# Kernel optimization log

Hardware: AMD Instinct MI355X
Metric: run time of the kernel (lower is better)

Reference implementation:

```python
import jax, jax.numpy as jnp
import numpy as np
import math

B, S, D = 2, 2048, 512
H = 8
DEPTH = D // H
MAX_REL = 1024
NEG_INF = -1.0e9


def skew(t):
    # t: (..., r, c). Pad a zero column on the left, reshape to move relative
    # logits into their absolute positions (Music Transformer skew trick).
    r, c = t.shape[-2], t.shape[-1]
    padded = jnp.pad(t, [(0, 0)] * (t.ndim - 1) + [(1, 0)])
    s = padded.reshape(-1, c + 1, r)[:, 1:]
    return s.reshape(t.shape)


def setup_inputs() -> dict:
    key = jax.random.key(0)
    ks = jax.random.split(key, 12)
    sc = 1.0 / math.sqrt(D)
    return {
        "q": jax.random.normal(ks[0], (B, S, D), jnp.float32),
        "k": jax.random.normal(ks[1], (B, S, D), jnp.float32),
        "v": jax.random.normal(ks[2], (B, S, D), jnp.float32),
        "mask": jax.random.randint(ks[3], (B, 1, S, S), 0, 2, jnp.int32),
        "Wq_w": jax.random.normal(ks[4], (D, D), jnp.float32) * sc,
        "Wq_b": jnp.zeros((D,), jnp.float32),
        "Wk_w": jax.random.normal(ks[5], (D, D), jnp.float32) * sc,
        "Wk_b": jnp.zeros((D,), jnp.float32),
        "Wv_w": jax.random.normal(ks[6], (D, D), jnp.float32) * sc,
        "Wv_b": jnp.zeros((D,), jnp.float32),
        "E": jax.random.normal(ks[7], (MAX_REL, D), jnp.float32),
        "Wo_w": jax.random.normal(ks[8], (D, D), jnp.float32) * sc,
        "Wo_b": jnp.zeros((D,), jnp.float32),
    }


def reference(q, k, v, mask, Wq_w, Wq_b, Wk_w, Wk_b, Wv_w, Wv_b, E, Wo_w, Wo_b):
    # Linear projections (torch Linear: x @ W^T + b)
    qp = q @ Wq_w.T + Wq_b
    kp = k @ Wk_w.T + Wk_b
    vp = v @ Wv_w.T + Wv_b

    # Required relative position embeddings for seq_len S (S >= MAX_REL here:
    # repeat E[0] for the first S-MAX_REL positions, then the full table).
    n_rep = max(0, S - MAX_REL)
    e = jnp.concatenate([jnp.tile(E[0:1], (n_rep, 1)), E[max(0, MAX_REL - S):]], axis=0)  # (S, D)

    # Split heads: (B,S,D)->(B,H,S,depth); e: (S,D)->(H,S,depth)
    qh = qp.reshape(B, S, H, DEPTH).transpose(0, 2, 1, 3)
    kh = kp.reshape(B, S, H, DEPTH).transpose(0, 2, 1, 3)
    vh = vp.reshape(B, S, H, DEPTH).transpose(0, 2, 1, 3)
    eh = e.reshape(S, H, DEPTH).transpose(1, 0, 2)

    QKt = jnp.einsum('bhqd,bhkd->bhqk', qh, kh)
    Srel = skew(jnp.einsum('bhqd,hkd->bhqk', qh, eh))
    logits = (QKt + Srel) / math.sqrt(DEPTH)
    logits = logits + mask.astype(logits.dtype) * NEG_INF
    attn = jnp.einsum('bhqk,bhkd->bhqd', jax.nn.softmax(logits, axis=-1), vh)

    # Merge heads and output projection
    out = attn.transpose(0, 2, 1, 3).reshape(B, S, D)
    return out @ Wo_w.T + Wo_b
```

## Files before the change

kernel.cpp:

```cpp
#include <hip/hip_runtime.h>
#include <hip/hip_bf16.h>

#define BB 2
#define SS 2048
#define DD 512
#define HH 8
#define DP 64
#define MR 1024

typedef __attribute__((ext_vector_type(8))) short bf16x8;
typedef __attribute__((ext_vector_type(4))) float floatx4;

static __device__ __forceinline__ unsigned short f2b(float x) {
    __hip_bfloat16 h = __float2bfloat16(x);
    return *reinterpret_cast<unsigned short*>(&h);
}
static __device__ __forceinline__ float b2f(unsigned short u) {
    __hip_bfloat16 h = *reinterpret_cast<__hip_bfloat16*>(&u);
    return __bfloat162float(h);
}
static __device__ __forceinline__ void gll16(const void* g, void* l) {
    __builtin_amdgcn_global_load_lds(
        (const __attribute__((address_space(1))) void*)g,
        (__attribute__((address_space(3))) void*)l, 16, 0, 0);
}
static __device__ __forceinline__ int xoff(int ks, int quad, int row) {
    return (((ks * 4 + quad) ^ (row & 7)) * 16);
}

__global__ __launch_bounds__(256) void prep_kernel(
    const float* __restrict__ Wq, const float* __restrict__ Wk,
    const float* __restrict__ Wv, const float* __restrict__ Wo,
    const float* __restrict__ E,  const float* __restrict__ q,
    const float* __restrict__ k,  const float* __restrict__ v,
    const int* __restrict__ mask,
    unsigned short* __restrict__ Wqb, unsigned short* __restrict__ Wkb,
    unsigned short* __restrict__ Wvb, unsigned short* __restrict__ Wob,
    unsigned short* __restrict__ Eb,  unsigned short* __restrict__ qb16,
    unsigned short* __restrict__ kb16, unsigned short* __restrict__ vb16,
    unsigned long long* __restrict__ bits)
{
    const int blk = blockIdx.x;
    if (blk < 7680) {
        const int gid = blk * 256 + threadIdx.x;
        const float* src; unsigned short* dst; int off;
        if      (gid < 65536)   { src = Wq; dst = Wqb;  off = gid; }
        else if (gid < 131072)  { src = Wk; dst = Wkb;  off = gid - 65536; }
        else if (gid < 196608)  { src = Wv; dst = Wvb;  off = gid - 131072; }
        else if (gid < 262144)  { src = Wo; dst = Wob;  off = gid - 196608; }
        else if (gid < 393216)  { src = E;  dst = Eb;   off = gid - 262144; }
        else if (gid < 917504)  { src = q;  dst = qb16; off = gid - 393216; }
        else if (gid < 1441792) { src = k;  dst = kb16; off = gid - 917504; }
        else                    { src = v;  dst = vb16; off = gid - 1441792; }
        float4 x = ((const float4*)src)[off];
        ushort4 u; u.x = f2b(x.x); u.y = f2b(x.y); u.z = f2b(x.z); u.w = f2b(x.w);
        ((ushort4*)dst)[off] = u;
    } else {
        const size_t wid = (size_t)(blk - 7680) * 4 + (threadIdx.x >> 6);
        const int lane = threadIdx.x & 63;
        const int mv = mask[wid * 64 + lane];
        unsigned long long bal = __ballot(mv != 0);
        if (lane == 0) bits[wid] = bal;
    }
}

__global__ __launch_bounds__(256) void gemm_proj(
    const unsigned short* __restrict__ Xq, const unsigned short* __restrict__ Xk,
    const unsigned short* __restrict__ Xv,
    const unsigned short* __restrict__ Wqb, const unsigned short* __restrict__ Wkb,
    const unsigned short* __restrict__ Wvb,
    const float* __restrict__ bq, const float* __restrict__ bk,
    const float* __restrict__ bv,
    unsigned short* __restrict__ qp, unsigned short* __restrict__ kp,
    unsigned short* __restrict__ vpT)
{
    const int z = blockIdx.z;
    const unsigned short* A  = (z == 0) ? Xq : (z == 1) ? Xk : Xv;
    const unsigned short* Wb = (z == 0) ? Wqb : (z == 1) ? Wkb : Wvb;
    const float* bias        = (z == 0) ? bq : (z == 1) ? bk : bv;

    __shared__ __align__(16) char parena[16384];
    char* AsB = parena;
    char* WsB = parena + 8192;
    const int t = threadIdx.x, lane = t & 63, w = t >> 6;
    const int quad = lane >> 4, l15 = lane & 15;
    const int wm = w >> 1, wn = w & 1;
    const int m0 = blockIdx.x * 64, n0 = blockIdx.y * 64;

    int srow[2], scol[2];
#pragma unroll
    for (int i = 0; i < 2; i++) {
        const int p = (w * 2 + i) * 64 + lane;
        srow[i] = p >> 3; scol[i] = (p & 7) ^ (srow[i] & 7);
    }

    floatx4 acc[2][2];
#pragma unroll
    for (int mi = 0; mi < 2; mi++)
#pragma unroll
        for (int ni = 0; ni < 2; ni++)
            acc[mi][ni] = (floatx4){0.f, 0.f, 0.f, 0.f};

    for (int k0 = 0; k0 < 512; k0 += 64) {
        if (k0) __syncthreads();
#pragma unroll
        for (int i = 0; i < 2; i++) {
            gll16(A + (size_t)(m0 + srow[i]) * 512 + k0 + scol[i] * 8,
                  AsB + (w * 2 + i) * 1024);
            gll16(Wb + (size_t)(n0 + srow[i]) * 512 + k0 + scol[i] * 8,
                  WsB + (w * 2 + i) * 1024);
        }
        __syncthreads();
#pragma unroll
        for (int ks = 0; ks < 2; ks++) {
            bf16x8 a[2], bb[2];
#pragma unroll
            for (int mi = 0; mi < 2; mi++) {
                const int row = wm * 32 + mi * 16 + l15;
                a[mi] = *(const bf16x8*)(AsB + row * 128 + xoff(ks, quad, row));
            }
#pragma unroll
            for (int ni = 0; ni < 2; ni++) {
                const int row = wn * 32 + ni * 16 + l15;
                bb[ni] = *(const bf16x8*)(WsB + row * 128 + xoff(ks, quad, row));
            }
#pragma unroll
            for (int mi = 0; mi < 2; mi++)
#pragma unroll
                for (int ni = 0; ni < 2; ni++)
                    acc[mi][ni] = __builtin_amdgcn_mfma_f32_16x16x32_bf16(
                        a[mi], bb[ni], acc[mi][ni], 0, 0, 0);
        }
    }

    if (z < 2) {
        unsigned short* Out = (z == 0) ? qp : kp;
#pragma unroll
        for (int ni = 0; ni < 2; ni++) {
            const int n = n0 + wn * 32 + ni * 16 + l15;
            const float bvl = bias[n];
#pragma unroll
            for (int mi = 0; mi < 2; mi++)
#pragma unroll
                for (int r = 0; r < 4; r++) {
                    const size_t m = (size_t)(m0 + wm * 32 + mi * 16 + quad * 4 + r);
                    Out[m * 512 + n] = f2b(acc[mi][ni][r] + bvl);
                }
        }
    } else {
        __syncthreads();
        unsigned short* Ls = (unsigned short*)parena;
#pragma unroll
        for (int ni = 0; ni < 2; ni++) {
            const int dcol = wn * 32 + ni * 16 + l15;
            const float bvl = bias[n0 + dcol];
#pragma unroll
            for (int mi = 0; mi < 2; mi++)
#pragma unroll
                for (int r = 0; r < 4; r++) {
                    const int srw = wm * 32 + mi * 16 + quad * 4 + r;
                    Ls[dcol * 72 + srw] = f2b(acc[mi][ni][r] + bvl);
                }
        }
        __syncthreads();
        const int bb2 = blockIdx.x >> 5, s0 = (blockIdx.x & 31) * 64, hh = blockIdx.y;
        const int drow = t >> 2, sc8 = (t & 3) * 8;
#pragma unroll
        for (int half = 0; half < 2; half++) {
            *(uint4*)&vpT[((size_t)(bb2 * 8 + hh) * 64 + drow) * SS + s0 + half * 32 + sc8] =
                *(const uint4*)&Ls[drow * 72 + half * 32 + sc8];
        }
    }
}

__global__ __launch_bounds__(256) void gemm_out(
    const unsigned short* __restrict__ A, const unsigned short* __restrict__ Wb,
    const float* __restrict__ bias, float* __restrict__ Out)
{
    __shared__ __align__(16) char parena[12288];
    char* AsB = parena;
    char* WsB = parena + 4096;
    const int t = threadIdx.x, lane = t & 63, w = t >> 6;
    const int quad = lane >> 4, l15 = lane & 15;
    const int wm = w >> 1, wn = w & 1;
    const int m0 = blockIdx.x * 32, n0 = blockIdx.y * 64;

    const int pa = w * 64 + lane;
    const int arow = pa >> 3, acol = (pa & 7) ^ (arow & 7);
    int wrow[2], wcol[2];
#pragma unroll
    for (int i = 0; i < 2; i++) {
        const int c = w * 2 + i;
        const int p = c * 64 + lane;
        wrow[i] = p >> 3; wcol[i] = (p & 7) ^ (wrow[i] & 7);
    }

    floatx4 acc[2];
    acc[0] = (floatx4){0.f, 0.f, 0.f, 0.f};
    acc[1] = (floatx4){0.f, 0.f, 0.f, 0.f};

    for (int k0 = 0; k0 < 512; k0 += 64) {
        if (k0) __syncthreads();
        gll16(A + (size_t)(m0 + arow) * 512 + k0 + acol * 8, AsB + w * 1024);
#pragma unroll
        for (int i = 0; i < 2; i++)
            gll16(Wb + (size_t)(n0 + wrow[i]) * 512 + k0 + wcol[i] * 8,
                  WsB + (w * 2 + i) * 1024);
        __syncthreads();
#pragma unroll
        for (int ks = 0; ks < 2; ks++) {
            bf16x8 a0 = *(const bf16x8*)(AsB + (wm * 16 + l15) * 128 + xoff(ks, quad, l15));
            bf16x8 b0 = *(const bf16x8*)(WsB + (wn * 32 + l15) * 128 + xoff(ks, quad, l15));
            bf16x8 b1 = *(const bf16x8*)(WsB + (wn * 32 + 16 + l15) * 128 + xoff(ks, quad, l15));
            acc[0] = __builtin_amdgcn_mfma_f32_16x16x32_bf16(a0, b0, acc[0], 0, 0, 0);
            acc[1] = __builtin_amdgcn_mfma_f32_16x16x32_bf16(a0, b1, acc[1], 0, 0, 0);
        }
    }
#pragma unroll
    for (int ct = 0; ct < 2; ct++) {
        const int n = n0 + wn * 32 + ct * 16 + l15;
        const float bvl = bias[n];
#pragma unroll
        for (int r = 0; r < 4; r++) {
            const size_t m = (size_t)(m0 + wm * 16 + quad * 4 + r);
            Out[m * 512 + n] = acc[ct][r] + bvl;
        }
    }
}

__global__ __launch_bounds__(256) void relg_kernel(
    const unsigned short* __restrict__ qp, const unsigned short* __restrict__ Eb,
    unsigned short* __restrict__ G)
{
    __shared__ unsigned short Ls[64 * 72];
    const int t = threadIdx.x, lane = t & 63, w = t >> 6;
    const int quad = lane >> 4, l15 = lane & 15;
    const int bh = blockIdx.z, b = bh >> 3, h = bh & 7;
    const int i0b = blockIdx.x * 64, t0 = blockIdx.y * 64;

    const unsigned short* Ar = qp + ((size_t)b * SS + i0b + w * 16 + l15) * DD + h * DP;
    bf16x8 a0 = *(const bf16x8*)(Ar + quad * 8);
    bf16x8 a1 = *(const bf16x8*)(Ar + 32 + quad * 8);

    floatx4 acc[4];
#pragma unroll
    for (int ct = 0; ct < 4; ct++) acc[ct] = (floatx4){0.f, 0.f, 0.f, 0.f};
#pragma unroll
    for (int ct = 0; ct < 4; ct++) {
        const unsigned short* Br = Eb + (size_t)(t0 + ct * 16 + l15) * DD + h * DP;
        bf16x8 b0 = *(const bf16x8*)(Br + quad * 8);
        bf16x8 b1 = *(const bf16x8*)(Br + 32 + quad * 8);
        acc[ct] = __builtin_amdgcn_mfma_f32_16x16x32_bf16(a0, b0, acc[ct], 0, 0, 0);
        acc[ct] = __builtin_amdgcn_mfma_f32_16x16x32_bf16(a1, b1, acc[ct], 0, 0, 0);
    }
#pragma unroll
    for (int ct = 0; ct < 4; ct++)
#pragma unroll
        for (int r = 0; r < 4; r++)
            Ls[(w * 16 + quad * 4 + r) * 72 + ct * 16 + l15] = f2b(acc[ct][r]);
    __syncthreads();
#pragma unroll
    for (int p = 0; p < 2; p++) {
        const int idx = p * 256 + t;
        const int row = idx >> 3, c8 = (idx & 7) * 8;
        *(uint4*)&G[((size_t)bh * SS + i0b + row) * MR + t0 + c8] =
            *(const uint4*)&Ls[row * 72 + c8];
    }
}

struct RelPF { ushort4 hi; ushort4 lo; int path; };

static __device__ __forceinline__ void rel_issue(
    const unsigned short* __restrict__ pdiag, int i0w, int k0, int quad,
    RelPF pf[2])
{
#pragma unroll
    for (int ct = 0; ct < 2; ct++) {
        const int k0c = k0 + ct * 16;
        const int gj0 = k0c + quad * 4;
        const int dmax = i0w + 15 - k0c;
        const int dmin = i0w - (k0c + 15);
        int path;
        if (dmin >= MR) path = 0;
        else if (dmin >= 0 && dmax <= MR - 1) path = 1;
        else if (dmax <= -2 && dmin >= -(MR + 1)) path = 2;
        else if (dmax <= -(MR + 2)) path = 3;
        else path = 4;
        pf[ct].path = path;
        if (path == 1 || path == 4) {
            const unsigned short* p = pdiag + 1023 + gj0;
            pf[ct].hi.x = p[0]; pf[ct].hi.y = p[1];
            pf[ct].hi.z = p[2]; pf[ct].hi.w = p[3];
        }
        if (path == 3 || path == 4) {
            const unsigned short* p = pdiag + max(gj0 - 2, 0);
            pf[ct].lo.x = p[0]; pf[ct].lo.y = p[1];
            pf[ct].lo.z = p[2]; pf[ct].lo.w = p[3];
        }
    }
}

static __device__ __forceinline__ void rel_convert(
    const RelPF& pf, int gi, int k0c, int quad,
    float d0a, float d0b, float relc[4])
{
    const int path = pf.path;
    if (path == 0) {
        relc[0] = relc[1] = relc[2] = relc[3] = d0a;
    } else if (path == 1) {
        relc[0] = b2f(pf.hi.x); relc[1] = b2f(pf.hi.y);
        relc[2] = b2f(pf.hi.z); relc[3] = b2f(pf.hi.w);
    } else if (path == 2) {
        relc[0] = relc[1] = relc[2] = relc[3] = d0b;
    } else if (path == 3) {
        relc[0] = b2f(pf.lo.x); relc[1] = b2f(pf.lo.y);
        relc[2] = b2f(pf.lo.z); relc[3] = b2f(pf.lo.w);
    } else {
        const int gj0 = k0c + quad * 4;
        const unsigned short hv[4] = {pf.hi.x, pf.hi.y, pf.hi.z, pf.hi.w};
        const unsigned short lv[4] = {pf.lo.x, pf.lo.y, pf.lo.z, pf.lo.w};
#pragma unroll
        for (int r = 0; r < 4; r++) {
            const int dd = gi - (gj0 + r);
            float rl;
            if (dd >= MR) rl = d0a;
            else if (dd >= 0) rl = b2f(hv[r]);
            else if (dd == -1) rl = 0.0f;
            else if (dd >= -(MR + 1)) rl = d0b;
            else rl = b2f(lv[r]);
            relc[r] = rl;
        }
    }
}

__global__ __launch_bounds__(256, 4) void attn_kernel(
    const unsigned short* __restrict__ qp, const unsigned short* __restrict__ kp,
    const unsigned short* __restrict__ vpT, const unsigned int* __restrict__ mb32,
    const unsigned short* __restrict__ G, unsigned short* __restrict__ ao)
{
    __shared__ __align__(16) char smem[38016];
    const int t = threadIdx.x, lane = t & 63, w = t >> 6;
    const int quad = lane >> 4, l15 = lane & 15;
    const int wr = w >> 1, kh = w & 1;
    const int bh = blockIdx.y, b = bh >> 3, h = bh & 7;
    const int i0w = blockIdx.x * 32 + wr * 16;
    const int gi = i0w + l15;

    const unsigned short* kb = kp + (size_t)b * SS * DD + h * DP;
    const unsigned short* vb = vpT + (size_t)bh * DP * SS;
    const unsigned short* Gb = G + (size_t)bh * SS * MR;
    const unsigned int* mrow32 = mb32 + ((size_t)b * SS + gi) * 64;

    const unsigned short* qrow = qp + ((size_t)b * SS + gi) * DD + h * DP;
    bf16x8 qf0 = *(const bf16x8*)(qrow + quad * 8);
    bf16x8 qf1 = *(const bf16x8*)(qrow + 32 + quad * 8);

    const unsigned short* pdiag = Gb + (size_t)gi * 1023;
    const float d0a = b2f(Gb[(size_t)gi * MR]);
    const float d0b = b2f(Gb[(size_t)min(gi + 1, SS - 1) * MR]);

    char* Kh = smem + kh * 8192;
    char* Vh = smem + 16384 + kh * 8192;
    char* Pt = smem + 32768 + w * 1280;

    int kofs[2], vofs[2], dst[2];
#pragma unroll
    for (int i = 0; i < 2; i++) {
        const int c = wr * 2 + i;
        const int p = c * 64 + lane;
        const int krow = p >> 3, kcol = (p & 7) ^ (krow & 7);
        kofs[i] = krow * DD + kcol * 8;
        const int vrow = p >> 2, vcol = (p & 3) ^ (vrow & 3);
        vofs[i] = vrow * SS + vcol * 8;
        dst[i] = c * 1024;
    }

    floatx4 oacc[4];
#pragma unroll
    for (int ct = 0; ct < 4; ct++) oacc[ct] = (floatx4){0.f, 0.f, 0.f, 0.f};
    float lsum = 0.0f;

    {
        const int k0 = kh * 1024;
        gll16(kb + (size_t)k0 * DD + kofs[0], Kh + dst[0]);
        gll16(kb + (size_t)k0 * DD + kofs[1], Kh + dst[1]);
        gll16(vb + k0 + vofs[0], Vh + dst[0]);
        gll16(vb + k0 + vofs[1], Vh + dst[1]);
    }
    unsigned int mwv = mrow32[kh * 32];
    RelPF pf[2];
    rel_issue(pdiag, i0w, kh * 1024, quad, pf);

    const float C1 = 0.125f * 1.4426950408889634f;
    const float C2 = -18.75f * 1.4426950408889634f;

    for (int it = 0; it < 32; it++) {
        const int cur = it & 1;
        __syncthreads();
        if (it + 1 < 32) {
            const int k0n = kh * 1024 + (it + 1) * 32;
            const int nb = (cur ^ 1) * 4096;
            gll16(kb + (size_t)k0n * DD + kofs[0], Kh + nb + dst[0]);
            gll16(kb + (size_t)k0n * DD + kofs[1], Kh + nb + dst[1]);
            gll16(vb + k0n + vofs[0], Vh + nb + dst[0]);
            gll16(vb + k0n + vofs[1], Vh + nb + dst[1]);
        }
        const unsigned int mcur = mwv;

        float relc[2][4];
        rel_convert(pf[0], gi, kh * 1024 + it * 32,      quad, d0a, d0b, relc[0]);
        rel_convert(pf[1], gi, kh * 1024 + it * 32 + 16, quad, d0a, d0b, relc[1]);

        {
            const int itn = (it + 1 < 32) ? it + 1 : 31;
            mwv = mrow32[kh * 32 + itn];
            rel_issue(pdiag, i0w, kh * 1024 + itn * 32, quad, pf);
        }

        char* Kc = Kh + cur * 4096;
        char* Vc = Vh + cur * 4096;

        bf16x8 kf[2][2];
#pragma unroll
        for (int ct = 0; ct < 2; ct++) {
            const int row = ct * 16 + l15;
            kf[ct][0] = *(const bf16x8*)(Kc + row * 128 + ((quad ^ (l15 & 7)) * 16));
            kf[ct][1] = *(const bf16x8*)(Kc + row * 128 + (((4 + quad) ^ (l15 & 7)) * 16));
        }
        bf16x8 vf[4];
#pragma unroll
        for (int ct = 0; ct < 4; ct++) {
            const int drow = ct * 16 + l15;
            vf[ct] = *(const bf16x8*)(Vc + drow * 64 + ((quad ^ (drow & 3)) * 16));
        }

        floatx4 acc[2];
#pragma unroll
        for (int ct = 0; ct < 2; ct++) {
            const unsigned int nib = (mcur >> (ct * 16 + quad * 4)) & 0xFu;
            floatx4 a;
#pragma unroll
            for (int r = 0; r < 4; r++)
                a[r] = relc[ct][r] + (((nib >> r) & 1u) ? -8.0e9f : 0.0f);
            acc[ct] = a;
        }
        __builtin_amdgcn_s_setprio(1);
#pragma unroll
        for (int ct = 0; ct < 2; ct++) {
            acc[ct] = __builtin_amdgcn_mfma_f32_16x16x32_bf16(kf[ct][0], qf0, acc[ct], 0, 0, 0);
            acc[ct] = __builtin_amdgcn_mfma_f32_16x16x32_bf16(kf[ct][1], qf1, acc[ct], 0, 0, 0);
        }
        __builtin_amdgcn_s_setprio(0);

#pragma unroll
        for (int ct = 0; ct < 2; ct++) {
            const float p0 = __builtin_exp2f(fmaf(acc[ct][0], C1, C2));
            const float p1 = __builtin_exp2f(fmaf(acc[ct][1], C1, C2));
            const float p2 = __builtin_exp2f(fmaf(acc[ct][2], C1, C2));
            const float p3 = __builtin_exp2f(fmaf(acc[ct][3], C1, C2));
            lsum += (p0 + p1) + (p2 + p3);
            ushort4 u;
            u.x = f2b(p0); u.y = f2b(p1); u.z = f2b(p2); u.w = f2b(p3);
            *(ushort4*)(Pt + l15 * 80 + ct * 32 + quad * 8) = u;
        }

        bf16x8 pt = *(const bf16x8*)(Pt + l15 * 80 + quad * 16);
        __builtin_amdgcn_s_setprio(1);
#pragma unroll
        for (int ct = 0; ct < 4; ct++)
            oacc[ct] = __builtin_amdgcn_mfma_f32_16x16x32_bf16(vf[ct], pt, oacc[ct], 0, 0, 0);
        __builtin_amdgcn_s_setprio(0);
    }

    lsum += __shfl_xor(lsum, 16);
    lsum += __shfl_xor(lsum, 32);

    __syncthreads();
    float* OmW = (float*)(smem + wr * 4352);
    float* MlW = (float*)(smem + 37888);
    if (kh == 1) {
#pragma unroll
        for (int ct = 0; ct < 4; ct++)
            *(floatx4*)&OmW[l15 * 68 + ct * 16 + quad * 4] = oacc[ct];
        if (lane < 16) MlW[wr * 16 + lane] = lsum;
    }
    __syncthreads();
    if (kh == 0) {
        const float inv = 1.0f / (lsum + MlW[wr * 16 + l15]);
#pragma unroll
        for (int ct = 0; ct < 4; ct++) {
            floatx4 o1 = *(const floatx4*)&OmW[l15 * 68 + ct * 16 + quad * 4];
            ushort4 u;
            u.x = f2b((oacc[ct][0] + o1[0]) * inv);
            u.y = f2b((oacc[ct][1] + o1[1]) * inv);
            u.z = f2b((oacc[ct][2] + o1[2]) * inv);
            u.w = f2b((oacc[ct][3] + o1[3]) * inv);
            *(ushort4*)&ao[((size_t)b * SS + gi) * DD + h * DP + ct * 16 + quad * 4] = u;
        }
    }
}

extern "C" void kernel_launch(void* const* d_in, const int* in_sizes, int n_in,
                              void* d_out, int out_size, void* d_ws, size_t ws_size,
                              hipStream_t stream)
{
    const float* q    = (const float*)d_in[0];
    const float* k    = (const float*)d_in[1];
    const float* v    = (const float*)d_in[2];
    const int*   mask = (const int*)d_in[3];
    const float* Wq_w = (const float*)d_in[4];
    const float* Wq_b = (const float*)d_in[5];
    const float* Wk_w = (const float*)d_in[6];
    const float* Wk_b = (const float*)d_in[7];
    const float* Wv_w = (const float*)d_in[8];
    const float* Wv_b = (const float*)d_in[9];
    const float* E    = (const float*)d_in[10];
    const float* Wo_w = (const float*)d_in[11];
    const float* Wo_b = (const float*)d_in[12];
    float* out = (float*)d_out;

    char* ws = (char*)d_ws;
    unsigned short* G    = (unsigned short*)ws;
    unsigned short* qp   = (unsigned short*)(ws + 67108864);
    unsigned short* kp   = qp + 2097152;
    unsigned short* vpT  = kp + 2 * 2097152;
    unsigned short* qb16 = vpT + 2097152;
    unsigned short* kb16 = qb16 + 2097152;
    unsigned short* vb16 = kb16 + 2097152;
    unsigned short* aob  = qb16;
    unsigned long long* mbits = (unsigned long long*)(ws + 67108864 + 7 * 4194304);
    unsigned short* Wqb = (unsigned short*)(ws + 67108864 + 7 * 4194304 + 1048576);
    unsigned short* Wkb = Wqb + 262144;
    unsigned short* Wvb = Wkb + 262144;
    unsigned short* Wob = Wvb + 262144;
    unsigned short* Ebf = Wob + 262144;

    dim3 blk(256);
    hipLaunchKernelGGL(prep_kernel, dim3(40448), blk, 0, stream,
                       Wq_w, Wk_w, Wv_w, Wo_w, E, q, k, v, mask,
                       Wqb, Wkb, Wvb, Wob, Ebf, qb16, kb16, vb16, mbits);
    hipLaunchKernelGGL(gemm_proj, dim3(64, 8, 3), blk, 0, stream,
                       qb16, kb16, vb16, Wqb, Wkb, Wvb, Wq_b, Wk_b, Wv_b,
                       qp, kp, vpT);
    hipLaunchKernelGGL(relg_kernel, dim3(32, 16, 16), blk, 0, stream, qp, Ebf, G);
    hipLaunchKernelGGL(attn_kernel, dim3(64, 16), blk, 0, stream,
                       qp, kp, vpT, (const unsigned int*)mbits, G, aob);
    hipLaunchKernelGGL(gemm_out, dim3(128, 8), blk, 0, stream, aob, Wob, Wo_b, out);
}
```

Before: 252.2 us.

## Fuse relative-logit GEMM into Q projection epilogue and enlarge output GEMM tiles

The separate relg_kernel is removed. Q-projection blocks now keep their bf16 Q tile in LDS and loop over all 16 E tiles to compute and write G directly, which saves one launch and the reread of qp. The output projection GEMM is rewritten to use 64x64 tiles, matching the projection kernel. In exchange, the z=0 blocks do a much longer serial loop than the K and V blocks, which creates load imbalance, and LDS use rises to about 27KB per block.

```diff
diff --git a/kernel.cpp b/kernel.cpp
--- a/kernel.cpp
+++ b/kernel.cpp
@@ -71,14 +71,169 @@
     const unsigned short* __restrict__ Wvb,
     const float* __restrict__ bq, const float* __restrict__ bk,
     const float* __restrict__ bv,
+    const unsigned short* __restrict__ Eb,
     unsigned short* __restrict__ qp, unsigned short* __restrict__ kp,
-    unsigned short* __restrict__ vpT)
+    unsigned short* __restrict__ vpT, unsigned short* __restrict__ G)
 {
     const int z = blockIdx.z;
     const unsigned short* A  = (z == 0) ? Xq : (z == 1) ? Xk : Xv;
     const unsigned short* Wb = (z == 0) ? Wqb : (z == 1) ? Wkb : Wvb;
     const float* bias        = (z == 0) ? bq : (z == 1) ? bk : bv;
 
+    __shared__ __align__(16) char parena[27648];
+    char* AsB = parena;
+    char* WsB = parena + 8192;
+    const int t = threadIdx.x, lane = t & 63, w = t >> 6;
+    const int quad = lane >> 4, l15 = lane & 15;
+    const int wm = w >> 1, wn = w & 1;
+    const int m0 = blockIdx.x * 64, n0 = blockIdx.y * 64;
+
+    int srow[2], scol[2];
+#pragma unroll
+    for (int i = 0; i < 2; i++) {
+        const int p = (w * 2 + i) * 64 + lane;
+        srow[i] = p >> 3; scol[i] = (p & 7) ^ (srow[i] & 7);
+    }
+
+    floatx4 acc[2][2];
+#pragma unroll
+    for (int mi = 0; mi < 2; mi++)
+#pragma unroll
+        for (int ni = 0; ni < 2; ni++)
+            acc[mi][ni] = (floatx4){0.f, 0.f, 0.f, 0.f};
+
+    for (int k0 = 0; k0 < 512; k0 += 64) {
+        if (k0) __syncthreads();
+#pragma unroll
+        for (int i = 0; i < 2; i++) {
+            gll16(A + (size_t)(m0 + srow[i]) * 512 + k0 + scol[i] * 8,
+                  AsB + (w * 2 + i) * 1024);
+            gll16(Wb + (size_t)(n0 + srow[i]) * 512 + k0 + scol[i] * 8,
+                  WsB + (w * 2 + i) * 1024);
+        }
+        __syncthreads();
+#pragma unroll
+        for (int ks = 0; ks < 2; ks++) {
+            bf16x8 a[2], bb[2];
+#pragma unroll
+            for (int mi = 0; mi < 2; mi++) {
+                const int row = wm * 32 + mi * 16 + l15;
+                a[mi] = *(const bf16x8*)(AsB + row * 128 + xoff(ks, quad, row));
+            }
+#pragma unroll
+            for (int ni = 0; ni < 2; ni++) {
+                const int row = wn * 32 + ni * 16 + l15;
+                bb[ni] = *(const bf16x8*)(WsB + row * 128 + xoff(ks, quad, row));
+            }
+#pragma unroll
+            for (int mi = 0; mi < 2; mi++)
+#pragma unroll
+                for (int ni = 0; ni < 2; ni++)
+                    acc[mi][ni] = __builtin_amdgcn_mfma_f32_16x16x32_bf16(
+                        a[mi], bb[ni], acc[mi][ni], 0, 0, 0);
+        }
+    }
+
+    if (z == 1) {
+#pragma unroll
+        for (int ni = 0; ni < 2; ni++) {
+            const int n = n0 + wn * 32 + ni * 16 + l15;
+            const float bvl = bias[n];
+#pragma unroll
+            for (int mi = 0; mi < 2; mi++)
+#pragma unroll
+                for (int r = 0; r < 4; r++) {
+                    const size_t m = (size_t)(m0 + wm * 32 + mi * 16 + quad * 4 + r);
+                    kp[m * 512 + n] = f2b(acc[mi][ni][r] + bvl);
+                }
+        }
+    } else if (z == 2) {
+        __syncthreads();
+        unsigned short* Ls = (unsigned short*)parena;
+#pragma unroll
+        for (int ni = 0; ni < 2; ni++) {
+            const int dcol = wn * 32 + ni * 16 + l15;
+            const float bvl = bias[n0 + dcol];
+#pragma unroll
+            for (int mi = 0; mi < 2; mi++)
+#pragma unroll
+                for (int r = 0; r < 4; r++) {
+                    const int srw = wm * 32 + mi * 16 + quad * 4 + r;
+                    Ls[dcol * 72 + srw] = f2b(acc[mi][ni][r] + bvl);
+                }
+        }
+        __syncthreads();
+        const int bb2 = blockIdx.x >> 5, s0 = (blockIdx.x & 31) * 64, hh = blockIdx.y;
+        const int drow = t >> 2, sc8 = (t & 3) * 8;
+#pragma unroll
+        for (int half = 0; half < 2; half++) {
+            *(uint4*)&vpT[((size_t)(bb2 * 8 + hh) * 64 + drow) * SS + s0 + half * 32 + sc8] =
+                *(const uint4*)&Ls[drow * 72 + half * 32 + sc8];
+        }
+    } else {
+        __syncthreads();
+        unsigned short* Ls = (unsigned short*)parena;
+#pragma unroll
+        for (int ni = 0; ni < 2; ni++) {
+            const int ch = wn * 32 + ni * 16 + l15;
+            const float bvl = bias[n0 + ch];
+#pragma unroll
+            for (int mi = 0; mi < 2; mi++)
+#pragma unroll
+                for (int r = 0; r < 4; r++)
+                    Ls[(wm * 32 + mi * 16 + quad * 4 + r) * 72 + ch] =
+                        f2b(acc[mi][ni][r] + bvl);
+        }
+        __syncthreads();
+        {
+            const int row = t >> 2, c16 = (t & 3) * 16;
+            const unsigned short* ls = &Ls[row * 72 + c16];
+            unsigned short* qdst = &qp[(size_t)(m0 + row) * 512 + n0 + c16];
+            *(uint4*)qdst = *(const uint4*)ls;
+            *(uint4*)(qdst + 8) = *(const uint4*)(ls + 8);
+        }
+        bf16x8 af0 = *(const bf16x8*)&Ls[(w * 16 + l15) * 72 + quad * 8];
+        bf16x8 af1 = *(const bf16x8*)&Ls[(w * 16 + l15) * 72 + 32 + quad * 8];
+
+        const int bblk = m0 >> 11;
+        const int i0 = m0 & 2047;
+        const size_t grow0 = (size_t)(bblk * 8 + blockIdx.y) * SS + i0;
+        char* EbL = parena + 10240;
+        unsigned short* Gtw = (unsigned short*)(parena + 18432 + w * 2304);
+
+        const int orow = lane >> 2, oseg = lane & 3;
+
+        for (int tc = 0; tc < 16; tc++) {
+            if (tc) __syncthreads();
+#pragma unroll
+            for (int i = 0; i < 2; i++)
+                gll16(Eb + (size_t)(tc * 64 + srow[i]) * 512 + n0 + scol[i] * 8,
+                      EbL + (w * 2 + i) * 1024);
+            __syncthreads();
+#pragma unroll
+            for (int tt = 0; tt < 4; tt++) {
+                const int row = tt * 16 + l15;
+                bf16x8 b0 = *(const bf16x8*)(EbL + row * 128 + xoff(0, quad, row));
+                bf16x8 b1 = *(const bf16x8*)(EbL + row * 128 + xoff(1, quad, row));
+                floatx4 a2 = (floatx4){0.f, 0.f, 0.f, 0.f};
+                a2 = __builtin_amdgcn_mfma_f32_16x16x32_bf16(af0, b0, a2, 0, 0, 0);
+                a2 = __builtin_amdgcn_mfma_f32_16x16x32_bf16(af1, b1, a2, 0, 0, 0);
+#pragma unroll
+                for (int r = 0; r < 4; r++)
+                    Gtw[(quad * 4 + r) * 72 + tt * 16 + l15] = f2b(a2[r]);
+            }
+            const unsigned short* gsrc = &Gtw[orow * 72 + oseg * 16];
+            unsigned short* gdst = &G[(grow0 + w * 16 + orow) * MR + tc * 64 + oseg * 16];
+            *(uint4*)gdst = *(const uint4*)gsrc;
+            *(uint4*)(gdst + 8) = *(const uint4*)(gsrc + 8);
+        }
+    }
+}
+
+__global__ __launch_bounds__(256) void gemm_out(
+    const unsigned short* __restrict__ A, const unsigned short* __restrict__ Wb,
+    const float* __restrict__ bias, float* __restrict__ Out)
+{
     __shared__ __align__(16) char parena[16384];
     char* AsB = parena;
     char* WsB = parena + 8192;
@@ -132,139 +287,17 @@
                         a[mi], bb[ni], acc[mi][ni], 0, 0, 0);
         }
     }
-
-    if (z < 2) {
-        unsigned short* Out = (z == 0) ? qp : kp;
-#pragma unroll
-        for (int ni = 0; ni < 2; ni++) {
-            const int n = n0 + wn * 32 + ni * 16 + l15;
-            const float bvl = bias[n];
-#pragma unroll
-            for (int mi = 0; mi < 2; mi++)
-#pragma unroll
-                for (int r = 0; r < 4; r++) {
-                    const size_t m = (size_t)(m0 + wm * 32 + mi * 16 + quad * 4 + r);
-                    Out[m * 512 + n] = f2b(acc[mi][ni][r] + bvl);
-                }
-        }
-    } else {
-        __syncthreads();
-        unsigned short* Ls = (unsigned short*)parena;
-#pragma unroll
-        for (int ni = 0; ni < 2; ni++) {
-            const int dcol = wn * 32 + ni * 16 + l15;
-            const float bvl = bias[n0 + dcol];
-#pragma unroll
-            for (int mi = 0; mi < 2; mi++)
-#pragma unroll
-                for (int r = 0; r < 4; r++) {
-                    const int srw = wm * 32 + mi * 16 + quad * 4 + r;
-                    Ls[dcol * 72 + srw] = f2b(acc[mi][ni][r] + bvl);
-                }
-        }
-        __syncthreads();
-        const int bb2 = blockIdx.x >> 5, s0 = (blockIdx.x & 31) * 64, hh = blockIdx.y;
-        const int drow = t >> 2, sc8 = (t & 3) * 8;
-#pragma unroll
-        for (int half = 0; half < 2; half++) {
-            *(uint4*)&vpT[((size_t)(bb2 * 8 + hh) * 64 + drow) * SS + s0 + half * 32 + sc8] =
-                *(const uint4*)&Ls[drow * 72 + half * 32 + sc8];
-        }
-    }
-}
-
-__global__ __launch_bounds__(256) void gemm_out(
-    const unsigned short* __restrict__ A, const unsigned short* __restrict__ Wb,
-    const float* __restrict__ bias, float* __restrict__ Out)
-{
-    __shared__ __align__(16) char parena[12288];
-    char* AsB = parena;
-    char* WsB = parena + 4096;
-    const int t = threadIdx.x, lane = t & 63, w = t >> 6;
-    const int quad = lane >> 4, l15 = lane & 15;
-    const int wm = w >> 1, wn = w & 1;
-    const int m0 = blockIdx.x * 32, n0 = blockIdx.y * 64;
-
-    const int pa = w * 64 + lane;
-    const int arow = pa >> 3, acol = (pa & 7) ^ (arow & 7);
-    int wrow[2], wcol[2];
-#pragma unroll
-    for (int i = 0; i < 2; i++) {
-        const int c = w * 2 + i;
-        const int p = c * 64 + lane;
-        wrow[i] = p >> 3; wcol[i] = (p & 7) ^ (wrow[i] & 7);
-    }
-
-    floatx4 acc[2];
-    acc[0] = (floatx4){0.f, 0.f, 0.f, 0.f};
-    acc[1] = (floatx4){0.f, 0.f, 0.f, 0.f};
-
-    for (int k0 = 0; k0 < 512; k0 += 64) {
-        if (k0) __syncthreads();
-        gll16(A + (size_t)(m0 + arow) * 512 + k0 + acol * 8, AsB + w * 1024);
-#pragma unroll
-        for (int i = 0; i < 2; i++)
-            gll16(Wb + (size_t)(n0 + wrow[i]) * 512 + k0 + wcol[i] * 8,
-                  WsB + (w * 2 + i) * 1024);
-        __syncthreads();
-#pragma unroll
-        for (int ks = 0; ks < 2; ks++) {
-            bf16x8 a0 = *(const bf16x8*)(AsB + (wm * 16 + l15) * 128 + xoff(ks, quad, l15));
-            bf16x8 b0 = *(const bf16x8*)(WsB + (wn * 32 + l15) * 128 + xoff(ks, quad, l15));
-            bf16x8 b1 = *(const bf16x8*)(WsB + (wn * 32 + 16 + l15) * 128 + xoff(ks, quad, l15));
-            acc[0] = __builtin_amdgcn_mfma_f32_16x16x32_bf16(a0, b0, acc[0], 0, 0, 0);
-            acc[1] = __builtin_amdgcn_mfma_f32_16x16x32_bf16(a0, b1, acc[1], 0, 0, 0);
-        }
-    }
-#pragma unroll
-    for (int ct = 0; ct < 2; ct++) {
-        const int n = n0 + wn * 32 + ct * 16 + l15;
+#pragma unroll
+    for (int ni = 0; ni < 2; ni++) {
+        const int n = n0 + wn * 32 + ni * 16 + l15;
         const float bvl = bias[n];
 #pragma unroll
-        for (int r = 0; r < 4; r++) {
-            const size_t m = (size_t)(m0 + wm * 16 + quad * 4 + r);
-            Out[m * 512 + n] = acc[ct][r] + bvl;
-        }
-    }
-}
-
-__global__ __launch_bounds__(256) void relg_kernel(
-    const unsigned short* __restrict__ qp, const unsigned short* __restrict__ Eb,
-    unsigned short* __restrict__ G)
-{
-    __shared__ unsigned short Ls[64 * 72];
-    const int t = threadIdx.x, lane = t & 63, w = t >> 6;
-    const int quad = lane >> 4, l15 = lane & 15;
-    const int bh = blockIdx.z, b = bh >> 3, h = bh & 7;
-    const int i0b = blockIdx.x * 64, t0 = blockIdx.y * 64;
-
-    const unsigned short* Ar = qp + ((size_t)b * SS + i0b + w * 16 + l15) * DD + h * DP;
-    bf16x8 a0 = *(const bf16x8*)(Ar + quad * 8);
-    bf16x8 a1 = *(const bf16x8*)(Ar + 32 + quad * 8);
-
-    floatx4 acc[4];
-#pragma unroll
-    for (int ct = 0; ct < 4; ct++) acc[ct] = (floatx4){0.f, 0.f, 0.f, 0.f};
-#pragma unroll
-    for (int ct = 0; ct < 4; ct++) {
-        const unsigned short* Br = Eb + (size_t)(t0 + ct * 16 + l15) * DD + h * DP;
-        bf16x8 b0 = *(const bf16x8*)(Br + quad * 8);
-        bf16x8 b1 = *(const bf16x8*)(Br + 32 + quad * 8);
-        acc[ct] = __builtin_amdgcn_mfma_f32_16x16x32_bf16(a0, b0, acc[ct], 0, 0, 0);
-        acc[ct] = __builtin_amdgcn_mfma_f32_16x16x32_bf16(a1, b1, acc[ct], 0, 0, 0);
-    }
-#pragma unroll
-    for (int ct = 0; ct < 4; ct++)
-#pragma unroll
-        for (int r = 0; r < 4; r++)
-            Ls[(w * 16 + quad * 4 + r) * 72 + ct * 16 + l15] = f2b(acc[ct][r]);
-    __syncthreads();
-#pragma unroll
-    for (int p = 0; p < 2; p++) {
-        const int idx = p * 256 + t;
-        const int row = idx >> 3, c8 = (idx & 7) * 8;
-        *(uint4*)&G[((size_t)bh * SS + i0b + row) * MR + t0 + c8] =
-            *(const uint4*)&Ls[row * 72 + c8];
+        for (int mi = 0; mi < 2; mi++)
+#pragma unroll
+            for (int r = 0; r < 4; r++) {
+                const size_t m = (size_t)(m0 + wm * 32 + mi * 16 + quad * 4 + r);
+                Out[m * 512 + n] = acc[mi][ni][r] + bvl;
+            }
     }
 }
 
@@ -541,9 +574,8 @@
                        Wqb, Wkb, Wvb, Wob, Ebf, qb16, kb16, vb16, mbits);
     hipLaunchKernelGGL(gemm_proj, dim3(64, 8, 3), blk, 0, stream,
                        qb16, kb16, vb16, Wqb, Wkb, Wvb, Wq_b, Wk_b, Wv_b,
-                       qp, kp, vpT);
-    hipLaunchKernelGGL(relg_kernel, dim3(32, 16, 16), blk, 0, stream, qp, Ebf, G);
+                       Ebf, qp, kp, vpT, G);
     hipLaunchKernelGGL(attn_kernel, dim3(64, 16), blk, 0, stream,
                        qp, kp, vpT, (const unsigned int*)mbits, G, aob);
-    hipLaunchKernelGGL(gemm_out, dim3(128, 8), blk, 0, stream, aob, Wob, Wo_b, out);
-}
+    hipLaunchKernelGGL(gemm_out, dim3(64, 8), blk, 0, stream, aob, Wob, Wo_b, out);
+}
```

Result: faster. 224.8 us (-10.9%).
